# Performance work log

Measured on AMD Instinct MI355X. Metric: run time of the kernel, lower is better.

## Reference

```python
import jax, jax.numpy as jnp
import numpy as np

D_MODEL = 1024
NUM_HEADS = 16
MODULUS = 2147483647
B, S = 2, 2048


def setup_inputs() -> dict:
    key = jax.random.key(0)
    d = D_MODEL
    names_dims = [
        ('q_w', d, d), ('k_w', d, d), ('v_w', d, d), ('o_w', d, d),
        ('emb1_w', 1, d // 2), ('emb2_w', d // 2, d),
        ('log_w', 1, d // 4), ('prime_w', 10, d // 4),
        ('div_w', 20, d // 4), ('bit_w', 32, d // 4),
        ('fus_w', d, d),
    ]
    ks = jax.random.split(key, len(names_dims) + 3)
    inp = {}
    for (name, fin, fout), k in zip(names_dims, ks[:len(names_dims)]):
        inp[name] = jax.random.normal(k, (fin, fout), jnp.float32) * 0.02
        inp[name.replace('_w', '_b')] = jnp.zeros((fout,), jnp.float32)
    inp['arith_bias'] = jax.random.normal(ks[-3], (NUM_HEADS, 1, 1), jnp.float32)
    inp['gcd_weight'] = jnp.ones((1,), jnp.float32)
    inp['encodings'] = jax.random.randint(ks[-2], (B, S), 1, 1000000, dtype=jnp.int32)
    return inp


def reference(encodings, q_w, q_b, k_w, k_b, v_w, v_b, o_w, o_b,
              emb1_w, emb1_b, emb2_w, emb2_b, log_w, log_b,
              prime_w, prime_b, div_w, div_b, bit_w, bit_b,
              fus_w, fus_b, arith_bias, gcd_weight):
    Bz, Sz = encodings.shape
    d = q_w.shape[0]
    H = NUM_HEADS
    hd = d // H

    # --- ArithmeticEmbedding ---
    ef = encodings.astype(jnp.float32)
    norm = (ef / MODULUS)[..., None]                       # [B,S,1]
    base = jnp.maximum(norm @ emb1_w + emb1_b, 0.0) @ emb2_w + emb2_b
    logf = jnp.log(ef + 1.0)[..., None] @ log_w + log_b    # [B,S,d/4]
    primes = jnp.array([2, 3, 5, 7, 11, 13, 17, 19, 23, 29], dtype=jnp.int32)
    pf = (encodings[..., None] % primes == 0).astype(jnp.float32) @ prime_w + prime_b
    tv = jnp.arange(2, 22, dtype=jnp.int32)
    df = ((encodings[..., None] % tv).astype(jnp.float32) / tv.astype(jnp.float32)) @ div_w + div_b
    shifts = jnp.arange(32, dtype=jnp.int32)
    bf = (((encodings[..., None] >> shifts) & 1)).astype(jnp.float32) @ bit_w + bit_b
    feats = jnp.concatenate([logf, pf, df, bf], axis=-1)   # [B,S,d]
    hidden = base + feats @ fus_w + fus_b

    # --- ArithmeticAttention ---
    q = (hidden @ q_w + q_b).reshape(Bz, Sz, H, hd)
    k = (hidden @ k_w + k_b).reshape(Bz, Sz, H, hd)
    v = (hidden @ v_w + v_b).reshape(Bz, Sz, H, hd)
    scores = jnp.einsum('bihd,bjhd->bhij', q, k) / jnp.sqrt(jnp.float32(hd))
    # vectorized arithmetic bias (original is an O(S^2) python loop)
    ei = encodings[:, :, None]
    ej = encodings[:, None, :]
    gcd_approx = jnp.minimum(ei % (ej + 1), ej % (ei + 1)).astype(jnp.float32)
    bias = gcd_approx / (jnp.maximum(ei, ej) + 1).astype(jnp.float32)
    bias = jnp.where(jnp.eye(Sz, dtype=bool)[None], 0.0, bias)  # i==j -> 0
    scores = scores + bias[:, None] * gcd_weight + arith_bias
    attn = jax.nn.softmax(scores, axis=-1)
    out = jnp.einsum('bhij,bjhd->bihd', attn, v).reshape(Bz, Sz, d)
    return out @ o_w + o_b
```

## Files before the change

### kernel.cpp

```cpp
#include <hip/hip_runtime.h>
#include <hip/hip_bf16.h>

typedef unsigned short u16;
typedef __attribute__((ext_vector_type(8))) __bf16 bf16x8;
typedef __attribute__((ext_vector_type(4))) float f32x4;

#define SEQ 2048
#define NB 2
#define NH 16
#define HD 64
#define DM 1024
#define LDQKV 3072
#define KF 576
#define LOG2E 1.4426950408889634f

__device__ __forceinline__ u16 f2bf(float f) {
    unsigned u = __float_as_uint(f);
    unsigned r = u + 0x7FFFu + ((u >> 16) & 1u);
    return (u16)(r >> 16);
}
__device__ __forceinline__ unsigned cvt_pk_bf16(float a, float b) {
    unsigned r;
    asm("v_cvt_pk_bf16_f32 %0, %1, %2" : "=v"(r) : "v"(a), "v"(b));
    return r;
}
__device__ __forceinline__ void gl_lds16(const u16* g, u16* l) {
    __builtin_amdgcn_global_load_lds((const __attribute__((address_space(1))) unsigned int*)g,
                                     (__attribute__((address_space(3))) unsigned int*)l, 16, 0, 0);
}

__global__ __launch_bounds__(256) void transw_kernel(const float* __restrict__ src,
                                                     u16* __restrict__ dst, int N, int ldd,
                                                     float scale) {
    __shared__ float tl[32][33];
    int tx = threadIdx.x, ty = threadIdx.y;
    int n = blockIdx.x * 32 + tx;
    int kbase = blockIdx.y * 32;
#pragma unroll
    for (int i = 0; i < 4; ++i)
        tl[ty + i * 8][tx] = src[(size_t)(kbase + ty + i * 8) * N + n];
    __syncthreads();
    int k = kbase + tx;
#pragma unroll
    for (int i = 0; i < 4; ++i) {
        int n2 = blockIdx.x * 32 + ty + i * 8;
        dst[(size_t)n2 * ldd + k] = f2bf(tl[tx][ty + i * 8] * scale);
    }
}

__global__ __launch_bounds__(256) void fold_kernel(const float* __restrict__ log_w,
                                                   const float* __restrict__ prime_w,
                                                   const float* __restrict__ div_w,
                                                   const float* __restrict__ bit_w,
                                                   const float* __restrict__ fus_w,
                                                   u16* __restrict__ WcT) {
    const int r = blockIdx.y;
    const int n = blockIdx.x * 256 + threadIdx.x;
    if (r == 63) { WcT[(size_t)n * KF + 575] = 0; return; }
    const float* wrow; int chunk;
    if (r == 0)       { wrow = log_w;                 chunk = 0;   }
    else if (r < 11)  { wrow = prime_w + (r - 1) * 256; chunk = 256; }
    else if (r < 31)  { wrow = div_w + (r - 11) * 256;  chunk = 512; }
    else              { wrow = bit_w + (r - 31) * 256;  chunk = 768; }
    float acc = 0.f;
#pragma unroll 8
    for (int m = 0; m < 256; ++m)
        acc += wrow[m] * fus_w[(size_t)(chunk + m) * DM + n];
    WcT[(size_t)n * KF + 512 + r] = f2bf(acc);
}

__global__ void cvec_kernel(const float* __restrict__ emb2_b, const float* __restrict__ fus_b,
                            const float* __restrict__ log_b, const float* __restrict__ prime_b,
                            const float* __restrict__ div_b, const float* __restrict__ bit_b,
                            const float* __restrict__ fus_w, float* __restrict__ cvec) {
    int n = blockIdx.x * 256 + threadIdx.x;
    float acc = emb2_b[n] + fus_b[n];
#pragma unroll 4
    for (int m = 0; m < 256; ++m) {
        acc += log_b[m]   * fus_w[(size_t)m * DM + n];
        acc += prime_b[m] * fus_w[(size_t)(256 + m) * DM + n];
        acc += div_b[m]   * fus_w[(size_t)(512 + m) * DM + n];
        acc += bit_b[m]   * fus_w[(size_t)(768 + m) * DM + n];
    }
    cvec[n] = acc;
}

__global__ void qkvb_kernel(const float* __restrict__ q_b, const float* __restrict__ k_b,
                            const float* __restrict__ v_b, float* __restrict__ qkvb) {
    int i = blockIdx.x * 256 + threadIdx.x;
    const float C1 = 0.125f * LOG2E;
    qkvb[i] = (i < 1024) ? q_b[i] * C1 : (i < 2048 ? k_b[i - 1024] : v_b[i - 2048]);
}

__global__ __launch_bounds__(256) void feat_kernel(const int* __restrict__ enc,
                                                   const float* __restrict__ emb1_w,
                                                   const float* __restrict__ emb1_b,
                                                   u16* __restrict__ F) {
    const int tok = blockIdx.x;
    const int t = threadIdx.x;
    int e = enc[tok];
    float ef = (float)e;
    float nrm = ef / 2147483647.0f;
    for (int k = t; k < 512; k += 256)
        F[(size_t)tok * KF + k] = f2bf(fmaxf(nrm * emb1_w[k] + emb1_b[k], 0.f));
    if (t < 64) {
        float v;
        if (t == 0) v = logf(ef + 1.f);
        else if (t < 11) {
            const int pr[10] = {2, 3, 5, 7, 11, 13, 17, 19, 23, 29};
            v = (e % pr[t - 1] == 0) ? 1.f : 0.f;
        } else if (t < 31) {
            int tv = t - 11 + 2;
            v = (float)(e % tv) / (float)tv;
        } else if (t < 63) {
            int sh = t - 31;
            v = (float)((e >> sh) & 1);
        } else v = 0.f;
        F[(size_t)tok * KF + 512 + t] = f2bf(v);
    }
}

template <int OUT_BF16, int TN>
__global__ __launch_bounds__(256) void gemm_kernel(const u16* __restrict__ A,
                                                   const u16* __restrict__ BT,
                                                   const float* __restrict__ bias,
                                                   void* __restrict__ Cv,
                                                   int M, int N, int K) {
    constexpr int FN = TN / 32;
    __shared__ u16 As[128 * 32];
    __shared__ u16 Bs[TN * 32];
    const int t = threadIdx.x;
    const int w = t >> 6, l = t & 63, lr = l & 15, lg = l >> 4;
    const int m0 = blockIdx.y * 128, n0 = blockIdx.x * TN;
    const int wm = (w >> 1) * 64, wn = (w & 1) * (TN / 2);
    const int srow = l >> 2, scol = (l & 3) * 8;

    const u16* gA = &A[(size_t)(m0 + w * 32 + srow) * K + scol];
    u16* lA = &As[w * 1024];
    const u16* gB;
    u16* lB;
    if (TN == 128) { gB = &BT[(size_t)(n0 + w * 32 + srow) * K + scol]; lB = &Bs[w * 1024]; }
    else           { gB = &BT[(size_t)(n0 + w * 16 + srow) * K + scol]; lB = &Bs[w * 512];  }

    f32x4 acc[4][FN] = {};
    for (int k0 = 0; k0 < K; k0 += 32) {
        __syncthreads();
        gl_lds16(gA + k0, lA);
        gl_lds16(gA + k0 + (size_t)16 * K, lA + 512);
        if (TN == 128) {
            gl_lds16(gB + k0, lB);
            gl_lds16(gB + k0 + (size_t)16 * K, lB + 512);
        } else {
            gl_lds16(gB + k0, lB);
        }
        __syncthreads();
        bf16x8 a[4], b[FN];
#pragma unroll
        for (int i = 0; i < 4; ++i) a[i] = *(const bf16x8*)&As[(wm + i * 16 + lr) * 32 + lg * 8];
#pragma unroll
        for (int j = 0; j < FN; ++j) b[j] = *(const bf16x8*)&Bs[(wn + j * 16 + lr) * 32 + lg * 8];
#pragma unroll
        for (int mi = 0; mi < 4; ++mi)
#pragma unroll
            for (int ni = 0; ni < FN; ++ni)
                acc[mi][ni] = __builtin_amdgcn_mfma_f32_16x16x32_bf16(a[mi], b[ni], acc[mi][ni], 0, 0, 0);
    }
#pragma unroll
    for (int mi = 0; mi < 4; ++mi)
#pragma unroll
        for (int ni = 0; ni < FN; ++ni)
#pragma unroll
            for (int r = 0; r < 4; ++r) {
                int row = m0 + wm + mi * 16 + lg * 4 + r;
                int col = n0 + wn + ni * 16 + lr;
                float v = acc[mi][ni][r] + bias[col];
                if (OUT_BF16)
                    ((u16*)Cv)[(size_t)row * N + col] = f2bf(v);
                else
                    ((float*)Cv)[(size_t)row * N + col] = v;
            }
}

__global__ __launch_bounds__(256) void vtrans_kernel(const u16* __restrict__ qkv,
                                                     u16* __restrict__ vT) {
    __shared__ u16 tile[64][72];
    int t = threadIdx.x;
    int s0 = blockIdx.x * 64, h = blockIdx.y, b = blockIdx.z;
    int sr = t >> 2, sc = (t & 3) * 16;
    const int4* g = (const int4*)&qkv[(size_t)(b * SEQ + s0 + sr) * LDQKV + 2048 + h * HD + sc];
    int4 v0 = g[0], v1 = g[1];
    *(int4*)&tile[sr][sc] = v0;
    *(int4*)&tile[sr][sc + 8] = v1;
    __syncthreads();
    int dl = sr, j0 = sc;
    u16 tmp[16];
#pragma unroll
    for (int jj = 0; jj < 16; ++jj) tmp[jj] = tile[j0 + jj][dl];
    u16* out = &vT[(size_t)((b * NH + h) * HD + dl) * SEQ + s0 + j0];
    *(int4*)&out[0] = *(int4*)&tmp[0];
    *(int4*)&out[8] = *(int4*)&tmp[8];
}

__global__ __launch_bounds__(256) void biasm_kernel(const int* __restrict__ enc,
                                                    const float* __restrict__ gcd_w,
                                                    float* __restrict__ biasMf) {
    int j = blockIdx.x * 256 + threadIdx.x;
    int i = blockIdx.y;
    int b = blockIdx.z;
    unsigned ei = (unsigned)enc[b * SEQ + i];
    unsigned ej = (unsigned)enc[b * SEQ + j];
    unsigned r1 = ei % (ej + 1u);
    unsigned r2 = ej % (ei + 1u);
    unsigned g = min(r1, r2);
    unsigned mx = max(ei, ej) + 1u;
    float v = (i == j) ? 0.f : (float)g / (float)mx;
    biasMf[((size_t)b * SEQ + i) * SEQ + j] = v * (gcd_w[0] * LOG2E);
}

#define KVB 64
#define SWZ(row, cb) ((((int)(row)) << 7) + (((int)(cb)) ^ ((((int)(row)) & 7) << 4)))

__global__ __launch_bounds__(256) void attn_kernel(const u16* __restrict__ qkv,
                                                   const u16* __restrict__ vT,
                                                   const float* __restrict__ biasMf,
                                                   u16* __restrict__ attn_out) {
    __shared__ char smem[40960];
    const int t = threadIdx.x, w = t >> 6, l = t & 63, lr = l & 15, lg = l >> 4;
    char* PlB = smem + 32768 + (w << 11);
    const int qt = blockIdx.x, h = blockIdx.y, b = blockIdx.z;
    const int qrow = qt * 64 + w * 16 + lr;

    bf16x8 qf[2];
#pragma unroll
    for (int kk = 0; kk < 2; ++kk)
        qf[kk] = *(const bf16x8*)&qkv[(size_t)(b * SEQ + qrow) * LDQKV + h * HD + kk * 32 + lg * 8];

    const int sr = t >> 2, sc = (t & 3) * 16;
    const u16* gK = &qkv[(size_t)(b * SEQ + sr) * LDQKV + 1024 + h * HD + sc];
    const u16* gV = &vT[(size_t)((b * NH + h) * HD + sr) * SEQ + sc];
    const float* gB = &biasMf[((size_t)b * SEQ + qrow) * SEQ + lg * 4];

    int4 kr0 = *(const int4*)&gK[0], kr1 = *(const int4*)&gK[8];
    int4 vr0 = *(const int4*)&gV[0], vr1 = *(const int4*)&gV[8];
    f32x4 br[4];
#pragma unroll
    for (int ni = 0; ni < 4; ++ni) br[ni] = *(const f32x4*)&gB[ni * 16];

    float m_s = -1e30f, l_s = 0.f;
    f32x4 acc_o[4] = {};

    for (int jt = 0; jt < SEQ / KVB; ++jt) {
        char* KtB = smem + (jt & 1) * 16384;
        char* VtB = KtB + 8192;
        *(int4*)(KtB + SWZ(sr, (t & 3) * 32))      = kr0;
        *(int4*)(KtB + SWZ(sr, (t & 3) * 32 + 16)) = kr1;
        *(int4*)(VtB + SWZ(sr, (t & 3) * 32))      = vr0;
        *(int4*)(VtB + SWZ(sr, (t & 3) * 32 + 16)) = vr1;
        const int jb2 = (jt + 1) * KVB;
        if (jt < SEQ / KVB - 1) {
            kr0 = *(const int4*)&gK[(size_t)jb2 * LDQKV];
            kr1 = *(const int4*)&gK[(size_t)jb2 * LDQKV + 8];
            vr0 = *(const int4*)&gV[jb2];
            vr1 = *(const int4*)&gV[jb2 + 8];
        }
        __syncthreads();

        f32x4 s[4];
#pragma unroll
        for (int ni = 0; ni < 4; ++ni) s[ni] = br[ni];
        if (jt < SEQ / KVB - 1) {
#pragma unroll
            for (int ni = 0; ni < 4; ++ni) br[ni] = *(const f32x4*)&gB[jb2 + ni * 16];
        }

#pragma unroll
        for (int kk = 0; kk < 2; ++kk)
#pragma unroll
            for (int ni = 0; ni < 4; ++ni) {
                bf16x8 kf = *(const bf16x8*)(KtB + SWZ(ni * 16 + lr, kk * 64 + lg * 16));
                s[ni] = __builtin_amdgcn_mfma_f32_16x16x32_bf16(kf, qf[kk], s[ni], 0, 0, 0);
            }

        float tm = s[0][0];
#pragma unroll
        for (int ni = 0; ni < 4; ++ni)
#pragma unroll
            for (int r = 0; r < 4; ++r) tm = fmaxf(tm, s[ni][r]);
        tm = fmaxf(tm, __shfl_xor(tm, 16));
        tm = fmaxf(tm, __shfl_xor(tm, 32));

        if (__any(tm > m_s + 8.f)) {
            float mn = fmaxf(m_s, tm);
            float al = __builtin_exp2f(m_s - mn);
            l_s *= al;
            m_s = mn;
#pragma unroll
            for (int nd = 0; nd < 4; ++nd)
#pragma unroll
                for (int r = 0; r < 4; ++r) acc_o[nd][r] *= al;
        }

        float ps = 0.f;
#pragma unroll
        for (int ni = 0; ni < 4; ++ni)
#pragma unroll
            for (int r = 0; r < 4; ++r) {
                float p = __builtin_exp2f(s[ni][r] - m_s);
                s[ni][r] = p;
                ps += p;
            }
        ps += __shfl_xor(ps, 16);
        ps += __shfl_xor(ps, 32);
        l_s += ps;

#pragma unroll
        for (int ni = 0; ni < 4; ++ni) {
            uint2 u;
            u.x = cvt_pk_bf16(s[ni][0], s[ni][1]);
            u.y = cvt_pk_bf16(s[ni][2], s[ni][3]);
            *(uint2*)(PlB + SWZ(lr, ni * 32 + lg * 8)) = u;
        }
        asm volatile("s_waitcnt lgkmcnt(0)" ::: "memory");
        __builtin_amdgcn_sched_barrier(0);

#pragma unroll
        for (int kc = 0; kc < 2; ++kc) {
            bf16x8 pf = *(const bf16x8*)(PlB + SWZ(lr, kc * 64 + lg * 16));
#pragma unroll
            for (int nd = 0; nd < 4; ++nd) {
                bf16x8 vf = *(const bf16x8*)(VtB + SWZ(nd * 16 + lr, kc * 64 + lg * 16));
                acc_o[nd] = __builtin_amdgcn_mfma_f32_16x16x32_bf16(vf, pf, acc_o[nd], 0, 0, 0);
            }
        }
    }

    float inv = 1.f / l_s;
    u16* orow = &attn_out[(size_t)(b * SEQ + qrow) * DM + h * HD];
#pragma unroll
    for (int nd = 0; nd < 4; ++nd) {
        uint2 u;
        u.x = cvt_pk_bf16(acc_o[nd][0] * inv, acc_o[nd][1] * inv);
        u.y = cvt_pk_bf16(acc_o[nd][2] * inv, acc_o[nd][3] * inv);
        *(uint2*)&orow[nd * 16 + lg * 4] = u;
    }
}

extern "C" void kernel_launch(void* const* d_in, const int* in_sizes, int n_in,
                              void* d_out, int out_size, void* d_ws, size_t ws_size,
                              hipStream_t stream) {
    const float* q_w    = (const float*)d_in[0];
    const float* q_b    = (const float*)d_in[1];
    const float* k_w    = (const float*)d_in[2];
    const float* k_b    = (const float*)d_in[3];
    const float* v_w    = (const float*)d_in[4];
    const float* v_b    = (const float*)d_in[5];
    const float* o_w    = (const float*)d_in[6];
    const float* o_b    = (const float*)d_in[7];
    const float* emb1_w = (const float*)d_in[8];
    const float* emb1_b = (const float*)d_in[9];
    const float* emb2_w = (const float*)d_in[10];
    const float* emb2_b = (const float*)d_in[11];
    const float* log_w  = (const float*)d_in[12];
    const float* log_b  = (const float*)d_in[13];
    const float* prime_w= (const float*)d_in[14];
    const float* prime_b= (const float*)d_in[15];
    const float* div_w  = (const float*)d_in[16];
    const float* div_b  = (const float*)d_in[17];
    const float* bit_w  = (const float*)d_in[18];
    const float* bit_b  = (const float*)d_in[19];
    const float* fus_w  = (const float*)d_in[20];
    const float* fus_b  = (const float*)d_in[21];
    const float* gcd_weight = (const float*)d_in[23];
    const int*   enc    = (const int*)d_in[24];

    char* ws = (char*)d_ws;
    size_t off = 0;
    auto alloc = [&](size_t bytes) {
        char* p = ws + off;
        off += (bytes + 255) & ~size_t(255);
        return p;
    };
    u16*   WcT    = (u16*)alloc((size_t)DM * KF * 2);
    u16*   WqkvT  = (u16*)alloc((size_t)3072 * DM * 2);
    u16*   WoT    = (u16*)alloc((size_t)DM * DM * 2);
    float* cvec   = (float*)alloc(DM * 4);
    float* qkvb   = (float*)alloc(3072 * 4);
    u16*   F      = (u16*)alloc((size_t)NB * SEQ * KF * 2);
    u16*   hidden = (u16*)alloc((size_t)NB * SEQ * DM * 2);
    u16*   qkv    = (u16*)alloc((size_t)NB * SEQ * LDQKV * 2);
    u16*   vT     = (u16*)alloc((size_t)NB * NH * HD * SEQ * 2);
    float* biasMf = (float*)alloc((size_t)NB * SEQ * SEQ * 4);
    u16*   attn_o = (u16*)alloc((size_t)NB * SEQ * DM * 2);
    (void)ws_size; (void)n_in; (void)in_sizes; (void)out_size;

    const float C1 = 0.125f * LOG2E;
    transw_kernel<<<dim3(32, 16), dim3(32, 8), 0, stream>>>(emb2_w, WcT, DM, KF, 1.0f);
    transw_kernel<<<dim3(32, 32), dim3(32, 8), 0, stream>>>(q_w, WqkvT, DM, DM, C1);
    transw_kernel<<<dim3(32, 32), dim3(32, 8), 0, stream>>>(k_w, WqkvT + (size_t)1024 * DM, DM, DM, 1.0f);
    transw_kernel<<<dim3(32, 32), dim3(32, 8), 0, stream>>>(v_w, WqkvT + (size_t)2048 * DM, DM, DM, 1.0f);
    transw_kernel<<<dim3(32, 32), dim3(32, 8), 0, stream>>>(o_w, WoT, DM, DM, 1.0f);
    fold_kernel<<<dim3(4, 64), 256, 0, stream>>>(log_w, prime_w, div_w, bit_w, fus_w, WcT);
    cvec_kernel<<<4, 256, 0, stream>>>(emb2_b, fus_b, log_b, prime_b, div_b, bit_b, fus_w, cvec);
    qkvb_kernel<<<12, 256, 0, stream>>>(q_b, k_b, v_b, qkvb);

    feat_kernel<<<NB * SEQ, 256, 0, stream>>>(enc, emb1_w, emb1_b, F);
    gemm_kernel<1, 64><<<dim3(DM / 64, NB * SEQ / 128), 256, 0, stream>>>(F, WcT, cvec, hidden,
                                                                          NB * SEQ, DM, KF);
    gemm_kernel<1, 128><<<dim3(3072 / 128, NB * SEQ / 128), 256, 0, stream>>>(hidden, WqkvT, qkvb, qkv,
                                                                              NB * SEQ, 3072, DM);
    vtrans_kernel<<<dim3(SEQ / 64, NH, NB), 256, 0, stream>>>(qkv, vT);
    biasm_kernel<<<dim3(SEQ / 256, SEQ, NB), 256, 0, stream>>>(enc, gcd_weight, biasMf);
    attn_kernel<<<dim3(SEQ / 64, NH, NB), 256, 0, stream>>>(qkv, vT, biasMf, attn_o);
    gemm_kernel<0, 64><<<dim3(DM / 64, NB * SEQ / 128), 256, 0, stream>>>(attn_o, WoT, o_b, d_out,
                                                                          NB * SEQ, DM, DM);
}
```

Baseline: 243.6 us.

## Fold embedding weights into QKV projection and split attention over KV halves

Precomputes a combined weight W2T = (Wc^T applied through WqkvT) so QKV is produced directly from the 576-wide feature matrix, which removes the hidden-state GEMM and its buffer. Attention is split into two KV halves along the grid with a separate combine kernel that merges the partial outputs using the saved max and sum statistics. This gives more blocks in flight at the cost of an extra pass and more memory traffic. The attention kernel also drops LDS double buffering in favour of a sync-then-store single buffer and adds s_setprio around the MFMA blocks. Rounding the folded weights and the partial outputs to bf16 adds precision risk.

```diff
diff --git a/kernel.cpp b/kernel.cpp
--- a/kernel.cpp
+++ b/kernel.cpp
@@ -13,11 +13,15 @@
 #define LDQKV 3072
 #define KF 576
 #define LOG2E 1.4426950408889634f
+#define NSPL 2
 
 __device__ __forceinline__ u16 f2bf(float f) {
     unsigned u = __float_as_uint(f);
     unsigned r = u + 0x7FFFu + ((u >> 16) & 1u);
     return (u16)(r >> 16);
+}
+__device__ __forceinline__ float bf2f(u16 x) {
+    return __uint_as_float(((unsigned)x) << 16);
 }
 __device__ __forceinline__ unsigned cvt_pk_bf16(float a, float b) {
     unsigned r;
@@ -48,15 +52,25 @@
     }
 }
 
+__global__ __launch_bounds__(256) void castwc_kernel(const float* __restrict__ src,
+                                                     u16* __restrict__ Wc) {
+    int i = (blockIdx.x * 256 + threadIdx.x) * 4;
+    float4 v = *(const float4*)&src[i];
+    uint2 o;
+    o.x = cvt_pk_bf16(v.x, v.y);
+    o.y = cvt_pk_bf16(v.z, v.w);
+    *(uint2*)&Wc[i] = o;
+}
+
 __global__ __launch_bounds__(256) void fold_kernel(const float* __restrict__ log_w,
                                                    const float* __restrict__ prime_w,
                                                    const float* __restrict__ div_w,
                                                    const float* __restrict__ bit_w,
                                                    const float* __restrict__ fus_w,
-                                                   u16* __restrict__ WcT) {
+                                                   u16* __restrict__ Wc) {
     const int r = blockIdx.y;
     const int n = blockIdx.x * 256 + threadIdx.x;
-    if (r == 63) { WcT[(size_t)n * KF + 575] = 0; return; }
+    if (r == 63) { Wc[(size_t)575 * DM + n] = 0; return; }
     const float* wrow; int chunk;
     if (r == 0)       { wrow = log_w;                 chunk = 0;   }
     else if (r < 11)  { wrow = prime_w + (r - 1) * 256; chunk = 256; }
@@ -66,7 +80,7 @@
 #pragma unroll 8
     for (int m = 0; m < 256; ++m)
         acc += wrow[m] * fus_w[(size_t)(chunk + m) * DM + n];
-    WcT[(size_t)n * KF + 512 + r] = f2bf(acc);
+    Wc[(size_t)(512 + r) * DM + n] = f2bf(acc);
 }
 
 __global__ void cvec_kernel(const float* __restrict__ emb2_b, const float* __restrict__ fus_b,
@@ -85,11 +99,17 @@
     cvec[n] = acc;
 }
 
-__global__ void qkvb_kernel(const float* __restrict__ q_b, const float* __restrict__ k_b,
-                            const float* __restrict__ v_b, float* __restrict__ qkvb) {
-    int i = blockIdx.x * 256 + threadIdx.x;
+__global__ void qkvb2_kernel(const float* __restrict__ q_b, const float* __restrict__ k_b,
+                             const float* __restrict__ v_b, const float* __restrict__ cvec,
+                             const u16* __restrict__ WqkvT, float* __restrict__ qkvb) {
+    int n = blockIdx.x * 256 + threadIdx.x;
     const float C1 = 0.125f * LOG2E;
-    qkvb[i] = (i < 1024) ? q_b[i] * C1 : (i < 2048 ? k_b[i - 1024] : v_b[i - 2048]);
+    float base = (n < 1024) ? q_b[n] * C1 : (n < 2048 ? k_b[n - 1024] : v_b[n - 2048]);
+    const u16* row = &WqkvT[(size_t)n * DM];
+    float acc = 0.f;
+#pragma unroll 8
+    for (int m = 0; m < DM; ++m) acc += cvec[m] * bf2f(row[m]);
+    qkvb[n] = base + acc;
 }
 
 __global__ __launch_bounds__(256) void feat_kernel(const int* __restrict__ enc,
@@ -120,7 +140,7 @@
     }
 }
 
-template <int OUT_BF16, int TN>
+template <int OUT_BF16, int TN, int HB>
 __global__ __launch_bounds__(256) void gemm_kernel(const u16* __restrict__ A,
                                                    const u16* __restrict__ BT,
                                                    const float* __restrict__ bias,
@@ -173,7 +193,7 @@
             for (int r = 0; r < 4; ++r) {
                 int row = m0 + wm + mi * 16 + lg * 4 + r;
                 int col = n0 + wn + ni * 16 + lr;
-                float v = acc[mi][ni][r] + bias[col];
+                float v = acc[mi][ni][r] + (HB ? bias[col] : 0.f);
                 if (OUT_BF16)
                     ((u16*)Cv)[(size_t)row * N + col] = f2bf(v);
                 else
@@ -223,12 +243,18 @@
 __global__ __launch_bounds__(256) void attn_kernel(const u16* __restrict__ qkv,
                                                    const u16* __restrict__ vT,
                                                    const float* __restrict__ biasMf,
-                                                   u16* __restrict__ attn_out) {
-    __shared__ char smem[40960];
+                                                   u16* __restrict__ Opart,
+                                                   float* __restrict__ Lp,
+                                                   float* __restrict__ Mp) {
+    __shared__ char smem[24576];
+    char* KtB = smem;
+    char* VtB = smem + 8192;
     const int t = threadIdx.x, w = t >> 6, l = t & 63, lr = l & 15, lg = l >> 4;
-    char* PlB = smem + 32768 + (w << 11);
-    const int qt = blockIdx.x, h = blockIdx.y, b = blockIdx.z;
+    char* PlB = smem + 16384 + (w << 11);
+    const int qt = blockIdx.x, h = blockIdx.y;
+    const int b = blockIdx.z >> 1, sp = blockIdx.z & 1;
     const int qrow = qt * 64 + w * 16 + lr;
+    const int j0 = sp * (SEQ / NSPL);
 
     bf16x8 qf[2];
 #pragma unroll
@@ -236,9 +262,9 @@
         qf[kk] = *(const bf16x8*)&qkv[(size_t)(b * SEQ + qrow) * LDQKV + h * HD + kk * 32 + lg * 8];
 
     const int sr = t >> 2, sc = (t & 3) * 16;
-    const u16* gK = &qkv[(size_t)(b * SEQ + sr) * LDQKV + 1024 + h * HD + sc];
-    const u16* gV = &vT[(size_t)((b * NH + h) * HD + sr) * SEQ + sc];
-    const float* gB = &biasMf[((size_t)b * SEQ + qrow) * SEQ + lg * 4];
+    const u16* gK = &qkv[(size_t)(b * SEQ + j0 + sr) * LDQKV + 1024 + h * HD + sc];
+    const u16* gV = &vT[(size_t)((b * NH + h) * HD + sr) * SEQ + j0 + sc];
+    const float* gB = &biasMf[((size_t)b * SEQ + qrow) * SEQ + j0 + lg * 4];
 
     int4 kr0 = *(const int4*)&gK[0], kr1 = *(const int4*)&gK[8];
     int4 vr0 = *(const int4*)&gV[0], vr1 = *(const int4*)&gV[8];
@@ -249,15 +275,15 @@
     float m_s = -1e30f, l_s = 0.f;
     f32x4 acc_o[4] = {};
 
-    for (int jt = 0; jt < SEQ / KVB; ++jt) {
-        char* KtB = smem + (jt & 1) * 16384;
-        char* VtB = KtB + 8192;
+    const int NT = SEQ / NSPL / KVB;
+    for (int lt = 0; lt < NT; ++lt) {
+        const int jb2 = (lt + 1) * KVB;
+        __syncthreads();
         *(int4*)(KtB + SWZ(sr, (t & 3) * 32))      = kr0;
         *(int4*)(KtB + SWZ(sr, (t & 3) * 32 + 16)) = kr1;
         *(int4*)(VtB + SWZ(sr, (t & 3) * 32))      = vr0;
         *(int4*)(VtB + SWZ(sr, (t & 3) * 32 + 16)) = vr1;
-        const int jb2 = (jt + 1) * KVB;
-        if (jt < SEQ / KVB - 1) {
+        if (lt < NT - 1) {
             kr0 = *(const int4*)&gK[(size_t)jb2 * LDQKV];
             kr1 = *(const int4*)&gK[(size_t)jb2 * LDQKV + 8];
             vr0 = *(const int4*)&gV[jb2];
@@ -266,20 +292,22 @@
         __syncthreads();
 
         f32x4 s[4];
-#pragma unroll
-        for (int ni = 0; ni < 4; ++ni) s[ni] = br[ni];
-        if (jt < SEQ / KVB - 1) {
+        __builtin_amdgcn_s_setprio(1);
+#pragma unroll
+        for (int ni = 0; ni < 4; ++ni) {
+            bf16x8 kf = *(const bf16x8*)(KtB + SWZ(ni * 16 + lr, lg * 16));
+            s[ni] = __builtin_amdgcn_mfma_f32_16x16x32_bf16(kf, qf[0], br[ni], 0, 0, 0);
+        }
+#pragma unroll
+        for (int ni = 0; ni < 4; ++ni) {
+            bf16x8 kf = *(const bf16x8*)(KtB + SWZ(ni * 16 + lr, 64 + lg * 16));
+            s[ni] = __builtin_amdgcn_mfma_f32_16x16x32_bf16(kf, qf[1], s[ni], 0, 0, 0);
+        }
+        __builtin_amdgcn_s_setprio(0);
+        if (lt < NT - 1) {
 #pragma unroll
             for (int ni = 0; ni < 4; ++ni) br[ni] = *(const f32x4*)&gB[jb2 + ni * 16];
         }
-
-#pragma unroll
-        for (int kk = 0; kk < 2; ++kk)
-#pragma unroll
-            for (int ni = 0; ni < 4; ++ni) {
-                bf16x8 kf = *(const bf16x8*)(KtB + SWZ(ni * 16 + lr, kk * 64 + lg * 16));
-                s[ni] = __builtin_amdgcn_mfma_f32_16x16x32_bf16(kf, qf[kk], s[ni], 0, 0, 0);
-            }
 
         float tm = s[0][0];
 #pragma unroll
@@ -323,6 +351,7 @@
         asm volatile("s_waitcnt lgkmcnt(0)" ::: "memory");
         __builtin_amdgcn_sched_barrier(0);
 
+        __builtin_amdgcn_s_setprio(1);
 #pragma unroll
         for (int kc = 0; kc < 2; ++kc) {
             bf16x8 pf = *(const bf16x8*)(PlB + SWZ(lr, kc * 64 + lg * 16));
@@ -332,17 +361,53 @@
                 acc_o[nd] = __builtin_amdgcn_mfma_f32_16x16x32_bf16(vf, pf, acc_o[nd], 0, 0, 0);
             }
         }
-    }
-
-    float inv = 1.f / l_s;
-    u16* orow = &attn_out[(size_t)(b * SEQ + qrow) * DM + h * HD];
+        __builtin_amdgcn_s_setprio(0);
+    }
+
+    u16* orow = &Opart[(size_t)((sp * NB + b) * SEQ + qrow) * DM + h * HD];
 #pragma unroll
     for (int nd = 0; nd < 4; ++nd) {
         uint2 u;
-        u.x = cvt_pk_bf16(acc_o[nd][0] * inv, acc_o[nd][1] * inv);
-        u.y = cvt_pk_bf16(acc_o[nd][2] * inv, acc_o[nd][3] * inv);
+        u.x = cvt_pk_bf16(acc_o[nd][0], acc_o[nd][1]);
+        u.y = cvt_pk_bf16(acc_o[nd][2], acc_o[nd][3]);
         *(uint2*)&orow[nd * 16 + lg * 4] = u;
     }
+    if (lg == 0) {
+        size_t idx = ((size_t)(sp * NB + b) * SEQ + qrow) * NH + h;
+        Lp[idx] = l_s;
+        Mp[idx] = m_s;
+    }
+}
+
+__global__ __launch_bounds__(256) void comb_kernel(const u16* __restrict__ Opart,
+                                                   const float* __restrict__ Lp,
+                                                   const float* __restrict__ Mp,
+                                                   u16* __restrict__ attn_o) {
+    int tid = blockIdx.x * 256 + threadIdx.x;
+    int base = tid * 4;
+    int b = base / (SEQ * DM);
+    int rem = base - b * SEQ * DM;
+    int i = rem / DM;
+    int c = rem - i * DM;
+    int h = c >> 6;
+    size_t ix1 = ((size_t)b * SEQ + i) * NH + h;
+    size_t ix2 = ((size_t)(NB + b) * SEQ + i) * NH + h;
+    float m1 = Mp[ix1], m2 = Mp[ix2];
+    float l1 = Lp[ix1], l2 = Lp[ix2];
+    float ms = fmaxf(m1, m2);
+    float a1 = __builtin_exp2f(m1 - ms), a2 = __builtin_exp2f(m2 - ms);
+    float inv = 1.f / (a1 * l1 + a2 * l2);
+    a1 *= inv; a2 *= inv;
+    uint2 o1 = *(const uint2*)&Opart[((size_t)b * SEQ + i) * DM + c];
+    uint2 o2 = *(const uint2*)&Opart[((size_t)(NB + b) * SEQ + i) * DM + c];
+    float v0 = a1 * bf2f(o1.x & 0xFFFF) + a2 * bf2f(o2.x & 0xFFFF);
+    float v1 = a1 * bf2f(o1.x >> 16)    + a2 * bf2f(o2.x >> 16);
+    float v2 = a1 * bf2f(o1.y & 0xFFFF) + a2 * bf2f(o2.y & 0xFFFF);
+    float v3 = a1 * bf2f(o1.y >> 16)    + a2 * bf2f(o2.y >> 16);
+    uint2 u;
+    u.x = cvt_pk_bf16(v0, v1);
+    u.y = cvt_pk_bf16(v2, v3);
+    *(uint2*)&attn_o[(size_t)(b * SEQ + i) * DM + c] = u;
 }
 
 extern "C" void kernel_launch(void* const* d_in, const int* in_sizes, int n_in,
@@ -380,37 +445,41 @@
         off += (bytes + 255) & ~size_t(255);
         return p;
     };
-    u16*   WcT    = (u16*)alloc((size_t)DM * KF * 2);
     u16*   WqkvT  = (u16*)alloc((size_t)3072 * DM * 2);
     u16*   WoT    = (u16*)alloc((size_t)DM * DM * 2);
+    u16*   Wc     = (u16*)alloc((size_t)KF * DM * 2);
+    u16*   W2T    = (u16*)alloc((size_t)3072 * KF * 2);
     float* cvec   = (float*)alloc(DM * 4);
     float* qkvb   = (float*)alloc(3072 * 4);
-    u16*   F      = (u16*)alloc((size_t)NB * SEQ * KF * 2);
-    u16*   hidden = (u16*)alloc((size_t)NB * SEQ * DM * 2);
     u16*   qkv    = (u16*)alloc((size_t)NB * SEQ * LDQKV * 2);
     u16*   vT     = (u16*)alloc((size_t)NB * NH * HD * SEQ * 2);
     float* biasMf = (float*)alloc((size_t)NB * SEQ * SEQ * 4);
     u16*   attn_o = (u16*)alloc((size_t)NB * SEQ * DM * 2);
+    u16*   Opart  = (u16*)alloc((size_t)NSPL * NB * SEQ * DM * 2);
+    float* Lp     = (float*)alloc((size_t)NSPL * NB * SEQ * NH * 4);
+    float* Mp     = (float*)alloc((size_t)NSPL * NB * SEQ * NH * 4);
+    u16*   F      = (u16*)biasMf;
     (void)ws_size; (void)n_in; (void)in_sizes; (void)out_size;
 
     const float C1 = 0.125f * LOG2E;
-    transw_kernel<<<dim3(32, 16), dim3(32, 8), 0, stream>>>(emb2_w, WcT, DM, KF, 1.0f);
     transw_kernel<<<dim3(32, 32), dim3(32, 8), 0, stream>>>(q_w, WqkvT, DM, DM, C1);
     transw_kernel<<<dim3(32, 32), dim3(32, 8), 0, stream>>>(k_w, WqkvT + (size_t)1024 * DM, DM, DM, 1.0f);
     transw_kernel<<<dim3(32, 32), dim3(32, 8), 0, stream>>>(v_w, WqkvT + (size_t)2048 * DM, DM, DM, 1.0f);
     transw_kernel<<<dim3(32, 32), dim3(32, 8), 0, stream>>>(o_w, WoT, DM, DM, 1.0f);
-    fold_kernel<<<dim3(4, 64), 256, 0, stream>>>(log_w, prime_w, div_w, bit_w, fus_w, WcT);
+    castwc_kernel<<<512, 256, 0, stream>>>(emb2_w, Wc);
+    fold_kernel<<<dim3(4, 64), 256, 0, stream>>>(log_w, prime_w, div_w, bit_w, fus_w, Wc);
     cvec_kernel<<<4, 256, 0, stream>>>(emb2_b, fus_b, log_b, prime_b, div_b, bit_b, fus_w, cvec);
-    qkvb_kernel<<<12, 256, 0, stream>>>(q_b, k_b, v_b, qkvb);
-
+    qkvb2_kernel<<<12, 256, 0, stream>>>(q_b, k_b, v_b, cvec, WqkvT, qkvb);
+
+    gemm_kernel<1, 64, 0><<<dim3(KF / 64, 3072 / 128), 256, 0, stream>>>(WqkvT, Wc, nullptr, W2T,
+                                                                         3072, KF, DM);
     feat_kernel<<<NB * SEQ, 256, 0, stream>>>(enc, emb1_w, emb1_b, F);
-    gemm_kernel<1, 64><<<dim3(DM / 64, NB * SEQ / 128), 256, 0, stream>>>(F, WcT, cvec, hidden,
-                                                                          NB * SEQ, DM, KF);
-    gemm_kernel<1, 128><<<dim3(3072 / 128, NB * SEQ / 128), 256, 0, stream>>>(hidden, WqkvT, qkvb, qkv,
-                                                                              NB * SEQ, 3072, DM);
+    gemm_kernel<1, 128, 1><<<dim3(3072 / 128, NB * SEQ / 128), 256, 0, stream>>>(F, W2T, qkvb, qkv,
+                                                                                 NB * SEQ, 3072, KF);
     vtrans_kernel<<<dim3(SEQ / 64, NH, NB), 256, 0, stream>>>(qkv, vT);
     biasm_kernel<<<dim3(SEQ / 256, SEQ, NB), 256, 0, stream>>>(enc, gcd_weight, biasMf);
-    attn_kernel<<<dim3(SEQ / 64, NH, NB), 256, 0, stream>>>(qkv, vT, biasMf, attn_o);
-    gemm_kernel<0, 64><<<dim3(DM / 64, NB * SEQ / 128), 256, 0, stream>>>(attn_o, WoT, o_b, d_out,
-                                                                          NB * SEQ, DM, DM);
-}
+    attn_kernel<<<dim3(SEQ / 64, NH, NB * NSPL), 256, 0, stream>>>(qkv, vT, biasMf, Opart, Lp, Mp);
+    comb_kernel<<<NB * SEQ * DM / 4 / 256, 256, 0, stream>>>(Opart, Lp, Mp, attn_o);
+    gemm_kernel<0, 64, 1><<<dim3(DM / 64, NB * SEQ / 128), 256, 0, stream>>>(attn_o, WoT, o_b, d_out,
+                                                                             NB * SEQ, DM, DM);
+}
```

New measurement: 272.6 us. 1.12x slower.

## Fold embedding weights into QKV GEMM, load K/V directly, fast-mod bias

Applied to the files above, without the earlier changes.

Multiplies the fused embedding weights Wc by the QKV weights once (a 3072x576 product), so the hidden activation GEMM disappears and QKV comes straight from the 576-wide feature matrix. The cvec bias is folded through the QKV weights into qkvb. The attention kernel drops its double-buffered LDS staging of K and V and reads MFMA operands straight from global memory with s_setprio, freeing LDS but relying on cache hits. The bias kernel swaps integer modulo for a float reciprocal based remainder with correction steps, which assumes the operands stay in the exactly representable float range.

```diff
diff --git a/kernel.cpp b/kernel.cpp
--- a/kernel.cpp
+++ b/kernel.cpp
@@ -19,6 +19,9 @@
     unsigned r = u + 0x7FFFu + ((u >> 16) & 1u);
     return (u16)(r >> 16);
 }
+__device__ __forceinline__ float bf2f(u16 x) {
+    return __uint_as_float(((unsigned)x) << 16);
+}
 __device__ __forceinline__ unsigned cvt_pk_bf16(float a, float b) {
     unsigned r;
     asm("v_cvt_pk_bf16_f32 %0, %1, %2" : "=v"(r) : "v"(a), "v"(b));
@@ -27,6 +30,13 @@
 __device__ __forceinline__ void gl_lds16(const u16* g, u16* l) {
     __builtin_amdgcn_global_load_lds((const __attribute__((address_space(1))) unsigned int*)g,
                                      (__attribute__((address_space(3))) unsigned int*)l, 16, 0, 0);
+}
+__device__ __forceinline__ unsigned fmod_u24(unsigned a, unsigned b) {
+    float q = truncf(__fdividef((float)a, (float)b));
+    int r = (int)a - (int)((unsigned)q * b);
+    r += (r < 0) ? (int)b : 0;
+    r -= (r >= (int)b) ? (int)b : 0;
+    return (unsigned)r;
 }
 
 __global__ __launch_bounds__(256) void transw_kernel(const float* __restrict__ src,
@@ -48,15 +58,25 @@
     }
 }
 
+__global__ __launch_bounds__(256) void castwc_kernel(const float* __restrict__ src,
+                                                     u16* __restrict__ Wc) {
+    int i = (blockIdx.x * 256 + threadIdx.x) * 4;
+    float4 v = *(const float4*)&src[i];
+    uint2 o;
+    o.x = cvt_pk_bf16(v.x, v.y);
+    o.y = cvt_pk_bf16(v.z, v.w);
+    *(uint2*)&Wc[i] = o;
+}
+
 __global__ __launch_bounds__(256) void fold_kernel(const float* __restrict__ log_w,
                                                    const float* __restrict__ prime_w,
                                                    const float* __restrict__ div_w,
                                                    const float* __restrict__ bit_w,
                                                    const float* __restrict__ fus_w,
-                                                   u16* __restrict__ WcT) {
+                                                   u16* __restrict__ Wc) {
     const int r = blockIdx.y;
     const int n = blockIdx.x * 256 + threadIdx.x;
-    if (r == 63) { WcT[(size_t)n * KF + 575] = 0; return; }
+    if (r == 63) { Wc[(size_t)575 * DM + n] = 0; return; }
     const float* wrow; int chunk;
     if (r == 0)       { wrow = log_w;                 chunk = 0;   }
     else if (r < 11)  { wrow = prime_w + (r - 1) * 256; chunk = 256; }
@@ -66,7 +86,7 @@
 #pragma unroll 8
     for (int m = 0; m < 256; ++m)
         acc += wrow[m] * fus_w[(size_t)(chunk + m) * DM + n];
-    WcT[(size_t)n * KF + 512 + r] = f2bf(acc);
+    Wc[(size_t)(512 + r) * DM + n] = f2bf(acc);
 }
 
 __global__ void cvec_kernel(const float* __restrict__ emb2_b, const float* __restrict__ fus_b,
@@ -85,11 +105,20 @@
     cvec[n] = acc;
 }
 
-__global__ void qkvb_kernel(const float* __restrict__ q_b, const float* __restrict__ k_b,
-                            const float* __restrict__ v_b, float* __restrict__ qkvb) {
-    int i = blockIdx.x * 256 + threadIdx.x;
+__global__ void qkvb2_kernel(const float* __restrict__ q_b, const float* __restrict__ k_b,
+                             const float* __restrict__ v_b, const float* __restrict__ cvec,
+                             const float* __restrict__ q_w, const float* __restrict__ k_w,
+                             const float* __restrict__ v_w, float* __restrict__ qkvb) {
+    int n = blockIdx.x * 256 + threadIdx.x;
     const float C1 = 0.125f * LOG2E;
-    qkvb[i] = (i < 1024) ? q_b[i] * C1 : (i < 2048 ? k_b[i - 1024] : v_b[i - 2048]);
+    int col = n & 1023;
+    const float* W = (n < 1024) ? q_w : (n < 2048 ? k_w : v_w);
+    float acc = 0.f;
+#pragma unroll 8
+    for (int m = 0; m < DM; ++m) acc += cvec[m] * W[(size_t)m * DM + col];
+    float base = (n < 1024) ? q_b[col] : (n < 2048 ? k_b[col] : v_b[col]);
+    float v = base + acc;
+    qkvb[n] = (n < 1024) ? v * C1 : v;
 }
 
 __global__ __launch_bounds__(256) void feat_kernel(const int* __restrict__ enc,
@@ -120,7 +149,7 @@
     }
 }
 
-template <int OUT_BF16, int TN>
+template <int OUT_BF16, int TN, int HB>
 __global__ __launch_bounds__(256) void gemm_kernel(const u16* __restrict__ A,
                                                    const u16* __restrict__ BT,
                                                    const float* __restrict__ bias,
@@ -173,7 +202,7 @@
             for (int r = 0; r < 4; ++r) {
                 int row = m0 + wm + mi * 16 + lg * 4 + r;
                 int col = n0 + wn + ni * 16 + lr;
-                float v = acc[mi][ni][r] + bias[col];
+                float v = acc[mi][ni][r] + (HB ? bias[col] : 0.f);
                 if (OUT_BF16)
                     ((u16*)Cv)[(size_t)row * N + col] = f2bf(v);
                 else
@@ -209,11 +238,11 @@
     int b = blockIdx.z;
     unsigned ei = (unsigned)enc[b * SEQ + i];
     unsigned ej = (unsigned)enc[b * SEQ + j];
-    unsigned r1 = ei % (ej + 1u);
-    unsigned r2 = ej % (ei + 1u);
-    unsigned g = min(r1, r2);
-    unsigned mx = max(ei, ej) + 1u;
-    float v = (i == j) ? 0.f : (float)g / (float)mx;
+    unsigned r1 = fmod_u24(ei, ej + 1u);
+    unsigned r2 = fmod_u24(ej, ei + 1u);
+    float g = (float)min(r1, r2);
+    float mx = (float)(max(ei, ej) + 1u);
+    float v = (i == j) ? 0.f : __fdividef(g, mx);
     biasMf[((size_t)b * SEQ + i) * SEQ + j] = v * (gcd_w[0] * LOG2E);
 }
 
@@ -224,9 +253,9 @@
                                                    const u16* __restrict__ vT,
                                                    const float* __restrict__ biasMf,
                                                    u16* __restrict__ attn_out) {
-    __shared__ char smem[40960];
+    __shared__ char smem[8192];
     const int t = threadIdx.x, w = t >> 6, l = t & 63, lr = l & 15, lg = l >> 4;
-    char* PlB = smem + 32768 + (w << 11);
+    char* PlB = smem + (w << 11);
     const int qt = blockIdx.x, h = blockIdx.y, b = blockIdx.z;
     const int qrow = qt * 64 + w * 16 + lr;
 
@@ -235,13 +264,10 @@
     for (int kk = 0; kk < 2; ++kk)
         qf[kk] = *(const bf16x8*)&qkv[(size_t)(b * SEQ + qrow) * LDQKV + h * HD + kk * 32 + lg * 8];
 
-    const int sr = t >> 2, sc = (t & 3) * 16;
-    const u16* gK = &qkv[(size_t)(b * SEQ + sr) * LDQKV + 1024 + h * HD + sc];
-    const u16* gV = &vT[(size_t)((b * NH + h) * HD + sr) * SEQ + sc];
+    const u16* pK = &qkv[((size_t)b * SEQ + lr) * LDQKV + 1024 + h * HD + lg * 8];
+    const u16* pV = &vT[((size_t)(b * NH + h) * HD + lr) * SEQ + lg * 8];
     const float* gB = &biasMf[((size_t)b * SEQ + qrow) * SEQ + lg * 4];
 
-    int4 kr0 = *(const int4*)&gK[0], kr1 = *(const int4*)&gK[8];
-    int4 vr0 = *(const int4*)&gV[0], vr1 = *(const int4*)&gV[8];
     f32x4 br[4];
 #pragma unroll
     for (int ni = 0; ni < 4; ++ni) br[ni] = *(const f32x4*)&gB[ni * 16];
@@ -250,36 +276,23 @@
     f32x4 acc_o[4] = {};
 
     for (int jt = 0; jt < SEQ / KVB; ++jt) {
-        char* KtB = smem + (jt & 1) * 16384;
-        char* VtB = KtB + 8192;
-        *(int4*)(KtB + SWZ(sr, (t & 3) * 32))      = kr0;
-        *(int4*)(KtB + SWZ(sr, (t & 3) * 32 + 16)) = kr1;
-        *(int4*)(VtB + SWZ(sr, (t & 3) * 32))      = vr0;
-        *(int4*)(VtB + SWZ(sr, (t & 3) * 32 + 16)) = vr1;
-        const int jb2 = (jt + 1) * KVB;
+        const int jb = jt * KVB;
+        f32x4 s[4];
+        const u16* pKt = pK + (size_t)jb * LDQKV;
+        __builtin_amdgcn_s_setprio(1);
+#pragma unroll
+        for (int ni = 0; ni < 4; ++ni) {
+            const u16* pr = pKt + (size_t)(ni * 16) * LDQKV;
+            bf16x8 k0 = *(const bf16x8*)pr;
+            bf16x8 k1 = *(const bf16x8*)(pr + 32);
+            s[ni] = __builtin_amdgcn_mfma_f32_16x16x32_bf16(k0, qf[0], br[ni], 0, 0, 0);
+            s[ni] = __builtin_amdgcn_mfma_f32_16x16x32_bf16(k1, qf[1], s[ni], 0, 0, 0);
+        }
+        __builtin_amdgcn_s_setprio(0);
         if (jt < SEQ / KVB - 1) {
-            kr0 = *(const int4*)&gK[(size_t)jb2 * LDQKV];
-            kr1 = *(const int4*)&gK[(size_t)jb2 * LDQKV + 8];
-            vr0 = *(const int4*)&gV[jb2];
-            vr1 = *(const int4*)&gV[jb2 + 8];
-        }
-        __syncthreads();
-
-        f32x4 s[4];
-#pragma unroll
-        for (int ni = 0; ni < 4; ++ni) s[ni] = br[ni];
-        if (jt < SEQ / KVB - 1) {
-#pragma unroll
-            for (int ni = 0; ni < 4; ++ni) br[ni] = *(const f32x4*)&gB[jb2 + ni * 16];
-        }
-
-#pragma unroll
-        for (int kk = 0; kk < 2; ++kk)
-#pragma unroll
-            for (int ni = 0; ni < 4; ++ni) {
-                bf16x8 kf = *(const bf16x8*)(KtB + SWZ(ni * 16 + lr, kk * 64 + lg * 16));
-                s[ni] = __builtin_amdgcn_mfma_f32_16x16x32_bf16(kf, qf[kk], s[ni], 0, 0, 0);
-            }
+#pragma unroll
+            for (int ni = 0; ni < 4; ++ni) br[ni] = *(const f32x4*)&gB[jb + KVB + ni * 16];
+        }
 
         float tm = s[0][0];
 #pragma unroll
@@ -323,15 +336,18 @@
         asm volatile("s_waitcnt lgkmcnt(0)" ::: "memory");
         __builtin_amdgcn_sched_barrier(0);
 
+        const u16* pVt = pV + jb;
+        __builtin_amdgcn_s_setprio(1);
 #pragma unroll
         for (int kc = 0; kc < 2; ++kc) {
             bf16x8 pf = *(const bf16x8*)(PlB + SWZ(lr, kc * 64 + lg * 16));
 #pragma unroll
             for (int nd = 0; nd < 4; ++nd) {
-                bf16x8 vf = *(const bf16x8*)(VtB + SWZ(nd * 16 + lr, kc * 64 + lg * 16));
+                bf16x8 vf = *(const bf16x8*)(pVt + (size_t)(nd * 16) * SEQ + kc * 32);
                 acc_o[nd] = __builtin_amdgcn_mfma_f32_16x16x32_bf16(vf, pf, acc_o[nd], 0, 0, 0);
             }
         }
+        __builtin_amdgcn_s_setprio(0);
     }
 
     float inv = 1.f / l_s;
@@ -380,13 +396,13 @@
         off += (bytes + 255) & ~size_t(255);
         return p;
     };
-    u16*   WcT    = (u16*)alloc((size_t)DM * KF * 2);
     u16*   WqkvT  = (u16*)alloc((size_t)3072 * DM * 2);
     u16*   WoT    = (u16*)alloc((size_t)DM * DM * 2);
+    u16*   Wc     = (u16*)alloc((size_t)KF * DM * 2);
+    u16*   W2T    = (u16*)alloc((size_t)3072 * KF * 2);
     float* cvec   = (float*)alloc(DM * 4);
     float* qkvb   = (float*)alloc(3072 * 4);
     u16*   F      = (u16*)alloc((size_t)NB * SEQ * KF * 2);
-    u16*   hidden = (u16*)alloc((size_t)NB * SEQ * DM * 2);
     u16*   qkv    = (u16*)alloc((size_t)NB * SEQ * LDQKV * 2);
     u16*   vT     = (u16*)alloc((size_t)NB * NH * HD * SEQ * 2);
     float* biasMf = (float*)alloc((size_t)NB * SEQ * SEQ * 4);
@@ -394,23 +410,23 @@
     (void)ws_size; (void)n_in; (void)in_sizes; (void)out_size;
 
     const float C1 = 0.125f * LOG2E;
-    transw_kernel<<<dim3(32, 16), dim3(32, 8), 0, stream>>>(emb2_w, WcT, DM, KF, 1.0f);
     transw_kernel<<<dim3(32, 32), dim3(32, 8), 0, stream>>>(q_w, WqkvT, DM, DM, C1);
     transw_kernel<<<dim3(32, 32), dim3(32, 8), 0, stream>>>(k_w, WqkvT + (size_t)1024 * DM, DM, DM, 1.0f);
     transw_kernel<<<dim3(32, 32), dim3(32, 8), 0, stream>>>(v_w, WqkvT + (size_t)2048 * DM, DM, DM, 1.0f);
     transw_kernel<<<dim3(32, 32), dim3(32, 8), 0, stream>>>(o_w, WoT, DM, DM, 1.0f);
-    fold_kernel<<<dim3(4, 64), 256, 0, stream>>>(log_w, prime_w, div_w, bit_w, fus_w, WcT);
+    castwc_kernel<<<512, 256, 0, stream>>>(emb2_w, Wc);
+    fold_kernel<<<dim3(4, 64), 256, 0, stream>>>(log_w, prime_w, div_w, bit_w, fus_w, Wc);
     cvec_kernel<<<4, 256, 0, stream>>>(emb2_b, fus_b, log_b, prime_b, div_b, bit_b, fus_w, cvec);
-    qkvb_kernel<<<12, 256, 0, stream>>>(q_b, k_b, v_b, qkvb);
-
+    qkvb2_kernel<<<12, 256, 0, stream>>>(q_b, k_b, v_b, cvec, q_w, k_w, v_w, qkvb);
+
+    gemm_kernel<1, 64, 0><<<dim3(KF / 64, 3072 / 128), 256, 0, stream>>>(WqkvT, Wc, nullptr, W2T,
+                                                                         3072, KF, DM);
     feat_kernel<<<NB * SEQ, 256, 0, stream>>>(enc, emb1_w, emb1_b, F);
-    gemm_kernel<1, 64><<<dim3(DM / 64, NB * SEQ / 128), 256, 0, stream>>>(F, WcT, cvec, hidden,
-                                                                          NB * SEQ, DM, KF);
-    gemm_kernel<1, 128><<<dim3(3072 / 128, NB * SEQ / 128), 256, 0, stream>>>(hidden, WqkvT, qkvb, qkv,
-                                                                              NB * SEQ, 3072, DM);
+    gemm_kernel<1, 128, 1><<<dim3(3072 / 128, NB * SEQ / 128), 256, 0, stream>>>(F, W2T, qkvb, qkv,
+                                                                                 NB * SEQ, 3072, KF);
     vtrans_kernel<<<dim3(SEQ / 64, NH, NB), 256, 0, stream>>>(qkv, vT);
     biasm_kernel<<<dim3(SEQ / 256, SEQ, NB), 256, 0, stream>>>(enc, gcd_weight, biasMf);
     attn_kernel<<<dim3(SEQ / 64, NH, NB), 256, 0, stream>>>(qkv, vT, biasMf, attn_o);
-    gemm_kernel<0, 64><<<dim3(DM / 64, NB * SEQ / 128), 256, 0, stream>>>(attn_o, WoT, o_b, d_out,
-                                                                          NB * SEQ, DM, DM);
-}
+    gemm_kernel<0, 64, 1><<<dim3(DM / 64, NB * SEQ / 128), 256, 0, stream>>>(attn_o, WoT, o_b, d_out,
+                                                                             NB * SEQ, DM, DM);
+}
```

Result: slower. 481.7 us (+97.7%).
